# Optimization experiments

Hardware: AMD Instinct MI355X
Metric: run time of the kernel (lower is better)

The kernel has to match this reference:

```python
import jax, jax.numpy as jnp
import numpy as np

B, N, D, E = 64, 512, 256, 128   # batch, n_nodes, node_model_dim, edge_model_dim
N_ITERS = 20                      # max_iter_sinkhorn with fixed_n_iters=True


def setup_inputs() -> dict:
    key = jax.random.key(0)
    ks = jax.random.split(key, 9)
    return {
        "node_embeddings_inputs": jax.random.normal(ks[0], (B, N, D), jnp.float32),
        "node_masks_inputs": jax.random.randint(ks[1], (B, N), 0, 2).astype(bool),
        "node_embeddings_outputs": jax.random.normal(ks[2], (B, N, D), jnp.float32),
        # learned parameters
        "node_padding_features": jax.random.normal(ks[3], (1, 1, D), jnp.float32),
        "positional_encoding_outputs": jax.random.normal(ks[4], (1, N, D), jnp.float32),
        # stand-in for the (externally defined) EvoformerSetMatching pair stack:
        # a bilinear pair-affinity head, followed by the module's own linear_aff
        "W_a": jax.random.normal(ks[5], (D, E), jnp.float32) / np.sqrt(D),
        "W_b": jax.random.normal(ks[6], (D, E), jnp.float32) / np.sqrt(D),
        "w_aff": jax.random.normal(ks[7], (E,), jnp.float32) / np.sqrt(E),  # linear_aff weight
        "b_aff": jnp.zeros((), jnp.float32),                                # linear_aff bias
    }


def _sinkhorn(K, n_iters):
    # Fixed-iteration Sinkhorn projection toward a doubly-stochastic matrix:
    # alternately normalize columns (dim=2 sums) and rows (dim=1 sums).
    def step(P, _):
        P = P / jnp.sum(P, axis=2, keepdims=True)  # row-normalize over inputs axis
        P = P / jnp.sum(P, axis=1, keepdims=True)  # col-normalize over outputs axis
        return P, None
    P, _ = jax.lax.scan(step, K, None, length=n_iters)
    return P


def reference(node_embeddings_inputs, node_masks_inputs, node_embeddings_outputs,
              node_padding_features, positional_encoding_outputs,
              W_a, W_b, w_aff, b_aff):
    # replace padded input nodes with the learned padding feature
    mask = node_masks_inputs[..., None]                              # [B, N, 1]
    x_in = jnp.where(mask, node_padding_features, node_embeddings_inputs)
    # add positional encoding to output nodes (add_positionnal_outputs=True)
    x_out = node_embeddings_outputs + positional_encoding_outputs

    # pairwise affinity: aff[b, i(out), j(in)]  (linear_aff fused into the contraction
    # so the [B,N,N,E] pair tensor is never materialized)
    a = (x_out @ W_a) * w_aff                                        # [B, N, E]
    b = x_in @ W_b                                                   # [B, N, E]
    aff = jnp.einsum('bie,bje->bij', a, b) + b_aff                   # [B, N, N]

    # approximate doubly-stochastic init: average of the two marginal softmaxes
    K = 0.5 * jax.nn.softmax(aff, axis=1) + 0.5 * jax.nn.softmax(aff, axis=2)
    return _sinkhorn(K, N_ITERS)
```

## Files before the change

### kernel.cpp

```cpp
#include <hip/hip_runtime.h>
#include <cstddef>

static constexpr int CB = 64;
static constexpr int CN = 512;
static constexpr int CD = 256;
static constexpr int CE = 128;
static constexpr int CIT = 20;

typedef _Float16 half_t;
typedef __attribute__((ext_vector_type(8))) _Float16 v8h;
typedef __attribute__((ext_vector_type(4))) _Float16 v4h;
typedef __attribute__((ext_vector_type(4))) float v4f;

__device__ __forceinline__ void store_dual(v4f* l2p, v4f* llcp, v4f v) {
  asm volatile("global_store_dwordx4 %0, %2, off sc0\n\t"
               "global_store_dwordx4 %1, %2, off sc0 sc1"
               :: "v"(l2p), "v"(llcp), "v"(v) : "memory");
}
__device__ __forceinline__ void poll6(const v4f* a0, const v4f* a1,
                                      const v4f* a2, const v4f* c0,
                                      const v4f* c1, const v4f* c2,
                                      v4f& x0, v4f& x1, v4f& x2,
                                      v4f& y0, v4f& y1, v4f& y2) {
  asm volatile("global_load_dwordx4 %0, %6, off sc0\n\t"
               "global_load_dwordx4 %1, %7, off sc0\n\t"
               "global_load_dwordx4 %2, %8, off sc0\n\t"
               "global_load_dwordx4 %3, %9, off sc0 sc1\n\t"
               "global_load_dwordx4 %4, %10, off sc0 sc1\n\t"
               "global_load_dwordx4 %5, %11, off sc0 sc1\n\t"
               "s_waitcnt vmcnt(0)"
               : "=&v"(x0), "=&v"(x1), "=&v"(x2),
                 "=&v"(y0), "=&v"(y1), "=&v"(y2)
               : "v"(a0), "v"(a1), "v"(a2), "v"(c0), "v"(c1), "v"(c2)
               : "memory");
}
__device__ __forceinline__ bool allpos(v4f v) {
  return v[0] > 0.0f && v[1] > 0.0f && v[2] > 0.0f && v[3] > 0.0f;
}

__global__ __launch_bounds__(512) void k0_init(
    const void* __restrict__ mask, int* __restrict__ flag,
    const float* __restrict__ W_a, const float* __restrict__ W_b,
    const float* __restrict__ w_aff,
    half_t* __restrict__ WaF, half_t* __restrict__ WbF,
    float4* __restrict__ clearp, int nclear4) {
  const int tid = threadIdx.x;
  const int blk = blockIdx.x;
  if (blk == 1) return;
  if (blk >= 18) {
    const int idx = (blk - 18) * 512 + tid;
    if (idx < nclear4)
      clearp[idx] = make_float4(-1.0f, -1.0f, -1.0f, -1.0f);
    return;
  }
  if (blk >= 2) {
    const bool is_a = (blk < 10);
    const float* W = is_a ? W_a : W_b;
    half_t* WF = is_a ? WaF : WbF;
    const int e = (blk - (is_a ? 2 : 10)) * 512 + tid;
    const int fB = e >> 6, lane = e & 63;
    const int nn = fB >> 3, kf = fB & 7;
    const int col = nn * 16 + (lane & 15);
    const int q = lane >> 4;
    const float scale = is_a ? w_aff[col] : 1.0f;
    v8h hv;
#pragma unroll
    for (int j = 0; j < 8; ++j) {
      const int k = kf * 32 + q * 8 + j;
      hv[j] = (half_t)(W[(size_t)k * CE + col] * scale);
    }
    *(v8h*)&WF[(size_t)e * 8] = hv;
    return;
  }
  __shared__ int cnt[5];
  if (tid < 5) cnt[tid] = 0;
  __syncthreads();
  const unsigned char* p = (const unsigned char*)mask;
  int l0 = 0, l1 = 0, l2 = 0, l3 = 0, l4 = 0;
  const int base = tid * 64;
  for (int k = 0; k < 64; ++k) {
    const int off = base + k;
    if (p[off]) {
      const int m4 = off & 3;
      if (m4 == 1) l1++;
      else if (m4 == 2) l2++;
      else if (m4 == 3) l3++;
      else if ((off & 7) == 4) l4++;
      else l0++;
    }
  }
  if (l0) atomicAdd(&cnt[0], 1);
  if (l1) atomicAdd(&cnt[1], 1);
  if (l2) atomicAdd(&cnt[2], 1);
  if (l3) atomicAdd(&cnt[3], 1);
  if (l4) atomicAdd(&cnt[4], 1);
  __syncthreads();
  if (tid == 0) {
    int f;
    if (cnt[1]) f = 1;
    else if (cnt[2] || cnt[3]) f = 2;
    else if (cnt[4]) f = 0;
    else if (cnt[0]) f = 3;
    else f = 1;
    *flag = f;
  }
}

__global__ __launch_bounds__(256) void prep_both(
    const float* __restrict__ out_emb, const float* __restrict__ pos,
    const float* __restrict__ in_emb, const float* __restrict__ pad,
    const void* __restrict__ maskp, const int* __restrict__ flagp,
    const half_t* __restrict__ WaF, const half_t* __restrict__ WbF,
    half_t* __restrict__ A_h, half_t* __restrict__ Bm_h) {
  __shared__ half_t Xs[64][264];
  const int tid = threadIdx.x;
  const int wv = tid >> 6, ln = tid & 63;
  const bool isA = blockIdx.x < 512;
  const int row0 = (isA ? blockIdx.x : blockIdx.x - 512) * 64;
  const float* X = isA ? out_emb : in_emb;
  const float* extra = isA ? pos : pad;
  const half_t* Wfrag = isA ? WaF : WbF;
  half_t* out = isA ? A_h : Bm_h;
  const int flag = isA ? 0 : *flagp;

#pragma unroll 4
  for (int it = 0; it < 16; ++it) {
    const int r = it * 4 + wv;
    const int row = row0 + r;
    const int c = ln * 4;
    float4 x4;
    if (isA) {
      x4 = *(const float4*)&X[(size_t)row * CD + c];
      const int i = row & (CN - 1);
      const float4 p4 = *(const float4*)&extra[(size_t)i * CD + c];
      x4.x += p4.x; x4.y += p4.y; x4.z += p4.z; x4.w += p4.w;
    } else {
      bool m;
      if (flag == 1)      m = ((const unsigned char*)maskp)[row] != 0;
      else if (flag == 2) m = ((const float*)maskp)[row] != 0.0f;
      else if (flag == 3) m = ((const long long*)maskp)[row] != 0;
      else                m = ((const int*)maskp)[row] != 0;
      if (m) x4 = *(const float4*)&extra[c];
      else   x4 = *(const float4*)&X[(size_t)row * CD + c];
    }
    v4h hv;
    hv[0] = (half_t)x4.x; hv[1] = (half_t)x4.y;
    hv[2] = (half_t)x4.z; hv[3] = (half_t)x4.w;
    *(v4h*)&Xs[r][c] = hv;
  }
  __syncthreads();

  const int q = ln >> 4, l = ln & 15;
  v8h af[8];
#pragma unroll
  for (int kf = 0; kf < 8; ++kf)
    af[kf] = *(v8h*)&Xs[wv * 16 + l][kf * 32 + q * 8];
  v4f acc[8] = {};
#pragma unroll
  for (int nn = 0; nn < 8; ++nn) {
    v8h bf[8];
#pragma unroll
    for (int kf = 0; kf < 8; ++kf)
      bf[kf] = *(const v8h*)&Wfrag[(size_t)((nn * 8 + kf) * 64 + ln) * 8];
#pragma unroll
    for (int kf = 0; kf < 8; ++kf)
      acc[nn] = __builtin_amdgcn_mfma_f32_16x16x32_f16(af[kf], bf[kf], acc[nn], 0, 0, 0);
  }
#pragma unroll
  for (int nn = 0; nn < 8; ++nn)
#pragma unroll
    for (int g = 0; g < 4; ++g) {
      const int row = row0 + wv * 16 + q * 4 + g;
      out[(size_t)row * CE + nn * 16 + l] = (half_t)acc[nn][g];
    }
}

__global__ __launch_bounds__(512, 2) void fused_reg(
    const half_t* __restrict__ A_h, const half_t* __restrict__ B_h,
    const float* __restrict__ baff, float* __restrict__ P,
    float* __restrict__ partInit, float* __restrict__ partIter,
    float* __restrict__ partInitL2, float* __restrict__ partIterL2) {
  __shared__ float comb2[8][512][2];
  __shared__ __align__(16) float2 w12[512];
  __shared__ __align__(16) float QsL[512];
  __shared__ __align__(16) v4f csinv4[128];
  __shared__ __align__(16) half_t wAll[1056];

  const int tid = threadIdx.x;
  const int wv = tid >> 6, ln = tid & 63;
  const int q = ln >> 4, l = ln & 15;
  const int b = blockIdx.x & 63;
  const int slab = blockIdx.x >> 6;
  const int i0 = slab * 128;
  const float bbs = *baff - 2.7725887f;

  int rs3[3];
  {
    int k = 0;
#pragma unroll
    for (int sl = 0; sl < 4; ++sl)
      if (sl != slab) rs3[k++] = sl;
  }

  v8h af[4];
  {
    const half_t* Arow = &A_h[((size_t)b * CN + i0 + wv * 16 + l) * CE];
#pragma unroll
    for (int ki = 0; ki < 4; ++ki)
      af[ki] = *(const v8h*)&Arow[ki * 32 + q * 8];
  }
  v4h eh[32];
  v4h ehT[32];
  const half_t* Bbase = &B_h[(size_t)b * CN * CE];
#pragma unroll
  for (int ct = 0; ct < 32; ++ct) {
    v8h bf[4];
    const half_t* Brow = &Bbase[(size_t)(ct * 16 + l) * CE];
#pragma unroll
    for (int ki = 0; ki < 4; ++ki)
      bf[ki] = *(const v8h*)&Brow[ki * 32 + q * 8];
    v4f acc = {}, accT = {};
#pragma unroll
    for (int ki = 0; ki < 4; ++ki) {
      acc  = __builtin_amdgcn_mfma_f32_16x16x32_f16(af[ki], bf[ki], acc,  0, 0, 0);
      accT = __builtin_amdgcn_mfma_f32_16x16x32_f16(bf[ki], af[ki], accT, 0, 0, 0);
    }
#pragma unroll
    for (int g = 0; g < 4; ++g) {
      eh[ct][g]  = (half_t)__expf(acc[g]  + bbs);
      ehT[ct][g] = (half_t)__expf(accT[g] + bbs);
    }
  }

  v4h ones;
  ones[0] = (half_t)1.0f; ones[1] = (half_t)1.0f;
  ones[2] = (half_t)1.0f; ones[3] = (half_t)1.0f;
  v4f rowacc0 = {}, rowacc1 = {};
#pragma unroll
  for (int ct = 0; ct < 32; ct += 2) {
    const v4f c0 = __builtin_amdgcn_mfma_f32_16x16x16f16(ones, eh[ct], (v4f){}, 0, 0, 0);
    const v4f c1 = __builtin_amdgcn_mfma_f32_16x16x16f16(ones, eh[ct + 1], (v4f){}, 0, 0, 0);
    if (ln < 16) {
      comb2[wv][ct * 16 + ln][0] = c0[0];
      comb2[wv][(ct + 1) * 16 + ln][0] = c1[0];
    }
    rowacc0 = __builtin_amdgcn_mfma_f32_16x16x16f16(ones, ehT[ct],     rowacc0, 0, 0, 0);
    rowacc1 = __builtin_amdgcn_mfma_f32_16x16x16f16(ones, ehT[ct + 1], rowacc1, 0, 0, 0);
  }
  const float rowtot = rowacc0[0] + rowacc1[0];
  float rv[4];
#pragma unroll
  for (int g = 0; g < 4; ++g)
    rv[g] = 1.0f / __shfl(rowtot, q * 4 + g);
  __syncthreads();

  {
    float S = 0.0f;
#pragma unroll
    for (int w = 0; w < 8; ++w) S += comb2[w][tid][0];
    QsL[tid] = S;
  }
  __syncthreads();
  if (tid < 128) {
    const v4f s4 = *(const v4f*)&QsL[tid * 4];
    v4f* piL = (v4f*)partInitL2 + (size_t)b * 4 * 128;
    v4f* piC = (v4f*)partInit   + (size_t)b * 4 * 128;
    store_dual(&piL[slab * 128 + tid], &piC[slab * 128 + tid], s4);
    const v4f* a0 = &piL[rs3[0] * 128 + tid];
    const v4f* a1 = &piL[rs3[1] * 128 + tid];
    const v4f* a2 = &piL[rs3[2] * 128 + tid];
    const v4f* c0 = &piC[rs3[0] * 128 + tid];
    const v4f* c1 = &piC[rs3[1] * 128 + tid];
    const v4f* c2 = &piC[rs3[2] * 128 + tid];
    v4f s0, s1, s2;
    bool g0 = false, g1 = false, g2 = false;
    while (true) {
      v4f x0, x1, x2, y0, y1, y2;
      poll6(a0, a1, a2, c0, c1, c2, x0, x1, x2, y0, y1, y2);
      if (!g0) { if (allpos(x0)) { s0 = x0; g0 = true; } else if (allpos(y0)) { s0 = y0; g0 = true; } }
      if (!g1) { if (allpos(x1)) { s1 = x1; g1 = true; } else if (allpos(y1)) { s1 = y1; g1 = true; } }
      if (!g2) { if (allpos(x2)) { s2 = x2; g2 = true; } else if (allpos(y2)) { s2 = y2; g2 = true; } }
      if (g0 && g1 && g2) break;
      __builtin_amdgcn_s_sleep(1);
    }
    const v4f T = s4 + s0 + s1 + s2;
    v4f ci;
    v4h w1v, w2v;
#pragma unroll
    for (int j = 0; j < 4; ++j) {
      ci[j] = 1.0f / T[j];
      w1v[j] = (half_t)(0.5f * ci[j]);
      w2v[j] = (half_t)1.0f;
    }
    csinv4[tid] = ci;
    *(v4h*)&wAll[tid * 4] = w1v;
    *(v4h*)&wAll[544 + tid * 4] = w2v;
  }
  __syncthreads();
  const float ci0 = ((const float*)csinv4)[tid];

  const half_t* wbase = (l == 1) ? (wAll + 544) : wAll;
  float u_[4], uri[4];
  for (int t = 0; t < CIT; ++t) {
    __syncthreads();
    v4f Pe = {}, Po = {};
#pragma unroll
    for (int ct = 0; ct < 32; ct += 2) {
      const v4h wf0 = *(const v4h*)&wbase[ct * 16 + q * 4];
      const v4h wf1 = *(const v4h*)&wbase[(ct + 1) * 16 + q * 4];
      Pe = __builtin_amdgcn_mfma_f32_16x16x16f16(wf0, ehT[ct],     Pe, 0, 0, 0);
      Po = __builtin_amdgcn_mfma_f32_16x16x16f16(wf1, ehT[ct + 1], Po, 0, 0, 0);
    }
    const float Prow1 = Pe[0] + Po[0];
    const float Prow2 = Pe[1] + Po[1];
    v4h u_h, uri_h;
#pragma unroll
    for (int g = 0; g < 4; ++g) {
      const float p1 = __shfl(Prow1, q * 4 + g);
      const float p2 = __shfl(Prow2, q * 4 + g);
      u_[g] = 1.0f / (p1 + 0.5f * rv[g] * p2);
      uri[g] = u_[g] * rv[g];
      u_h[g] = (half_t)u_[g];
      uri_h[g] = (half_t)uri[g];
    }
    const v4h a2 = (l == 1) ? uri_h : u_h;
#pragma unroll
    for (int ct = 0; ct < 32; ++ct) {
      const v4f s = __builtin_amdgcn_mfma_f32_16x16x16f16(a2, eh[ct], (v4f){}, 0, 0, 0);
      if (ln < 16)
        *(float2*)&comb2[wv][ct * 16 + ln][0] = make_float2(s[0], s[1]);
    }
    __syncthreads();
    {
      float S1 = 0.0f, S2 = 0.0f;
#pragma unroll
      for (int w = 0; w < 8; ++w) {
        const float2 c2v = *(const float2*)&comb2[w][tid][0];
        S1 += c2v.x;
        S2 += c2v.y;
      }
      QsL[tid] = 0.5f * fmaf(ci0, S1, S2);
    }
    __syncthreads();
    if (tid < 128) {
      const v4f Q4 = *(const v4f*)&QsL[tid * 4];
      v4f* prL = (v4f*)partIterL2 + (((size_t)t * 64 + b) * 4) * 128;
      v4f* prC = (v4f*)partIter   + (((size_t)t * 64 + b) * 4) * 128;
      store_dual(&prL[slab * 128 + tid], &prC[slab * 128 + tid], Q4);
      const v4f* a0 = &prL[rs3[0] * 128 + tid];
      const v4f* a1 = &prL[rs3[1] * 128 + tid];
      const v4f* a2p = &prL[rs3[2] * 128 + tid];
      const v4f* c0 = &prC[rs3[0] * 128 + tid];
      const v4f* c1 = &prC[rs3[1] * 128 + tid];
      const v4f* c2 = &prC[rs3[2] * 128 + tid];
      v4f s0, s1, s2;
      bool g0 = false, g1 = false, g2 = false;
      while (true) {
        v4f x0, x1, x2, y0, y1, y2;
        poll6(a0, a1, a2p, c0, c1, c2, x0, x1, x2, y0, y1, y2);
        if (!g0) { if (allpos(x0)) { s0 = x0; g0 = true; } else if (allpos(y0)) { s0 = y0; g0 = true; } }
        if (!g1) { if (allpos(x1)) { s1 = x1; g1 = true; } else if (allpos(y1)) { s1 = y1; g1 = true; } }
        if (!g2) { if (allpos(x2)) { s2 = x2; g2 = true; } else if (allpos(y2)) { s2 = y2; g2 = true; } }
        if (g0 && g1 && g2) break;
        __builtin_amdgcn_s_sleep(1);
      }
      const v4f tot = Q4 + s0 + s1 + s2;
      const v4f ci = csinv4[tid];
      v4h w1v, w2v;
#pragma unroll
      for (int j = 0; j < 4; ++j) {
        const float vv = 1.0f / tot[j];
        w1v[j] = (half_t)(0.5f * vv * ci[j]);
        w2v[j] = (half_t)vv;
        if (t == CIT - 1)
          w12[tid * 4 + j] = make_float2(0.5f * vv * ci[j], vv);
      }
      *(v4h*)&wAll[tid * 4] = w1v;
      *(v4h*)&wAll[544 + tid * 4] = w2v;
    }
  }

  __syncthreads();
  float* Pb = &P[((size_t)b * CN + i0 + wv * 16 + q * 4) * CN];
#pragma unroll
  for (int ct = 0; ct < 32; ++ct) {
    const float2 w = w12[ct * 16 + l];
    const float c1 = w.x;
    const float c2 = 0.5f * w.y;
#pragma unroll
    for (int g = 0; g < 4; ++g) {
      const float e = (float)eh[ct][g];
      Pb[(size_t)g * CN + ct * 16 + l] = e * fmaf(u_[g], c1, uri[g] * c2);
    }
  }
}

extern "C" void kernel_launch(void* const* d_in, const int* in_sizes, int n_in,
                              void* d_out, int out_size, void* d_ws, size_t ws_size,
                              hipStream_t stream) {
  const float* in_emb  = (const float*)d_in[0];
  const void*  mask    = d_in[1];
  const float* out_emb = (const float*)d_in[2];
  const float* pad     = (const float*)d_in[3];
  const float* pos     = (const float*)d_in[4];
  const float* W_a     = (const float*)d_in[5];
  const float* W_b     = (const float*)d_in[6];
  const float* w_aff   = (const float*)d_in[7];
  const float* b_aff   = (const float*)d_in[8];
  float* P = (float*)d_out;

  char* ws = (char*)d_ws;
  const size_t MB = 1024 * 1024;
  const size_t KB = 1024;
  half_t* A_h  = (half_t*)ws;
  half_t* Bm_h = (half_t*)(ws + 8 * MB);
  int*    flag = (int*)(ws + 16 * MB);
  half_t* WaF  = (half_t*)(ws + 16 * MB + 16 * KB);
  half_t* WbF  = (half_t*)(ws + 16 * MB + 80 * KB);
  float* partInit   = (float*)(ws + 16 * MB + 256 * KB);
  float* partInitL2 = (float*)(ws + 16 * MB + 768 * KB);
  float* partIter   = (float*)(ws + 16 * MB + 1280 * KB);
  float* partIterL2 = (float*)(ws + 16 * MB + 1280 * KB + 10 * MB);

  const int nclear4 = (21 * 1024 * 1024) / 16;
  const int nclrblk = (nclear4 + 511) / 512;

  k0_init<<<dim3(18 + nclrblk), dim3(512), 0, stream>>>(
      mask, flag, W_a, W_b, w_aff, WaF, WbF, (float4*)partInit, nclear4);
  prep_both<<<dim3(1024), dim3(256), 0, stream>>>(
      out_emb, pos, in_emb, pad, mask, flag, WaF, WbF, A_h, Bm_h);
  fused_reg<<<dim3(256), dim3(512), 0, stream>>>(
      A_h, Bm_h, b_aff, P, partInit, partIter, partInitL2, partIterL2);
}
```

Baseline: 323.9 us.

## Co-locate batch slabs on one XCD and ring-buffer LLC partials with sign parity

Block indices are remapped so the four slab blocks of each batch share blockIdx mod 8. That likely places them on the same XCD, so the L2-coherent path of the cross-block partial-sum exchange can succeed instead of falling back to the slower LLC path. The LLC copy of the per-iteration partials becomes a two-slot ring. The sign alternates every two iterations, so stale data from two steps earlier can be told apart from fresh data. This shrinks the workspace region that k0_init must clear from 21 MB to 12 MB. The cost is a sign multiply and a parity-dependent check in the polling loop, and the scheme relies on partial sums being strictly positive.

```diff
diff --git a/kernel.cpp b/kernel.cpp
--- a/kernel.cpp
+++ b/kernel.cpp
@@ -12,10 +12,11 @@
 typedef __attribute__((ext_vector_type(4))) _Float16 v4h;
 typedef __attribute__((ext_vector_type(4))) float v4f;
 
-__device__ __forceinline__ void store_dual(v4f* l2p, v4f* llcp, v4f v) {
+__device__ __forceinline__ void store_dual2(v4f* l2p, v4f* llcp, v4f vpos,
+                                            v4f vsgn) {
   asm volatile("global_store_dwordx4 %0, %2, off sc0\n\t"
-               "global_store_dwordx4 %1, %2, off sc0 sc1"
-               :: "v"(l2p), "v"(llcp), "v"(v) : "memory");
+               "global_store_dwordx4 %1, %3, off sc0 sc1"
+               :: "v"(l2p), "v"(llcp), "v"(vpos), "v"(vsgn) : "memory");
 }
 __device__ __forceinline__ void poll6(const v4f* a0, const v4f* a1,
                                       const v4f* a2, const v4f* c0,
@@ -36,6 +37,9 @@
 }
 __device__ __forceinline__ bool allpos(v4f v) {
   return v[0] > 0.0f && v[1] > 0.0f && v[2] > 0.0f && v[3] > 0.0f;
+}
+__device__ __forceinline__ bool allneg(v4f v) {
+  return v[0] < 0.0f && v[1] < 0.0f && v[2] < 0.0f && v[3] < 0.0f;
 }
 
 __global__ __launch_bounds__(512) void k0_init(
@@ -178,8 +182,8 @@
 __global__ __launch_bounds__(512, 2) void fused_reg(
     const half_t* __restrict__ A_h, const half_t* __restrict__ B_h,
     const float* __restrict__ baff, float* __restrict__ P,
-    float* __restrict__ partInit, float* __restrict__ partIter,
-    float* __restrict__ partInitL2, float* __restrict__ partIterL2) {
+    float* __restrict__ partInit, float* __restrict__ partInitL2,
+    float* __restrict__ partIter, float* __restrict__ partIterL2) {
   __shared__ float comb2[8][512][2];
   __shared__ __align__(16) float2 w12[512];
   __shared__ __align__(16) float QsL[512];
@@ -189,8 +193,10 @@
   const int tid = threadIdx.x;
   const int wv = tid >> 6, ln = tid & 63;
   const int q = ln >> 4, l = ln & 15;
-  const int b = blockIdx.x & 63;
-  const int slab = blockIdx.x >> 6;
+  const int xcd = blockIdx.x & 7;
+  const int j_ = blockIdx.x >> 3;
+  const int b = ((j_ >> 2) << 3) | xcd;
+  const int slab = j_ & 3;
   const int i0 = slab * 128;
   const float bbs = *baff - 2.7725887f;
 
@@ -265,7 +271,7 @@
     const v4f s4 = *(const v4f*)&QsL[tid * 4];
     v4f* piL = (v4f*)partInitL2 + (size_t)b * 4 * 128;
     v4f* piC = (v4f*)partInit   + (size_t)b * 4 * 128;
-    store_dual(&piL[slab * 128 + tid], &piC[slab * 128 + tid], s4);
+    store_dual2(&piL[slab * 128 + tid], &piC[slab * 128 + tid], s4, s4);
     const v4f* a0 = &piL[rs3[0] * 128 + tid];
     const v4f* a1 = &piL[rs3[1] * 128 + tid];
     const v4f* a2 = &piL[rs3[2] * 128 + tid];
@@ -344,9 +350,13 @@
     __syncthreads();
     if (tid < 128) {
       const v4f Q4 = *(const v4f*)&QsL[tid * 4];
+      const int buf = t & 1;
+      const bool neg = ((t >> 1) & 1) != 0;
+      const float sgn = neg ? -1.0f : 1.0f;
+      const v4f Qs = Q4 * sgn;
       v4f* prL = (v4f*)partIterL2 + (((size_t)t * 64 + b) * 4) * 128;
-      v4f* prC = (v4f*)partIter   + (((size_t)t * 64 + b) * 4) * 128;
-      store_dual(&prL[slab * 128 + tid], &prC[slab * 128 + tid], Q4);
+      v4f* prC = (v4f*)partIter   + (((size_t)buf * 64 + b) * 4) * 128;
+      store_dual2(&prL[slab * 128 + tid], &prC[slab * 128 + tid], Q4, Qs);
       const v4f* a0 = &prL[rs3[0] * 128 + tid];
       const v4f* a1 = &prL[rs3[1] * 128 + tid];
       const v4f* a2p = &prL[rs3[2] * 128 + tid];
@@ -358,9 +368,12 @@
       while (true) {
         v4f x0, x1, x2, y0, y1, y2;
         poll6(a0, a1, a2p, c0, c1, c2, x0, x1, x2, y0, y1, y2);
-        if (!g0) { if (allpos(x0)) { s0 = x0; g0 = true; } else if (allpos(y0)) { s0 = y0; g0 = true; } }
-        if (!g1) { if (allpos(x1)) { s1 = x1; g1 = true; } else if (allpos(y1)) { s1 = y1; g1 = true; } }
-        if (!g2) { if (allpos(x2)) { s2 = x2; g2 = true; } else if (allpos(y2)) { s2 = y2; g2 = true; } }
+        if (!g0) { if (allpos(x0)) { s0 = x0; g0 = true; }
+                   else if (neg ? allneg(y0) : allpos(y0)) { s0 = y0 * sgn; g0 = true; } }
+        if (!g1) { if (allpos(x1)) { s1 = x1; g1 = true; }
+                   else if (neg ? allneg(y1) : allpos(y1)) { s1 = y1 * sgn; g1 = true; } }
+        if (!g2) { if (allpos(x2)) { s2 = x2; g2 = true; }
+                   else if (neg ? allneg(y2) : allpos(y2)) { s2 = y2 * sgn; g2 = true; } }
         if (g0 && g1 && g2) break;
         __builtin_amdgcn_s_sleep(1);
       }
@@ -417,12 +430,13 @@
   int*    flag = (int*)(ws + 16 * MB);
   half_t* WaF  = (half_t*)(ws + 16 * MB + 16 * KB);
   half_t* WbF  = (half_t*)(ws + 16 * MB + 80 * KB);
-  float* partInit   = (float*)(ws + 16 * MB + 256 * KB);
-  float* partInitL2 = (float*)(ws + 16 * MB + 768 * KB);
-  float* partIter   = (float*)(ws + 16 * MB + 1280 * KB);
-  float* partIterL2 = (float*)(ws + 16 * MB + 1280 * KB + 10 * MB);
-
-  const int nclear4 = (21 * 1024 * 1024) / 16;
+  char* slots = ws + 16 * MB + 256 * KB;
+  float* partInit   = (float*)(slots);
+  float* partInitL2 = (float*)(slots + 512 * KB);
+  float* partIter   = (float*)(slots + 1 * MB);
+  float* partIterL2 = (float*)(slots + 2 * MB);
+
+  const int nclear4 = (12 * 1024 * 1024) / 16;
   const int nclrblk = (nclear4 + 511) / 512;
 
   k0_init<<<dim3(18 + nclrblk), dim3(512), 0, stream>>>(
@@ -430,5 +444,5 @@
   prep_both<<<dim3(1024), dim3(256), 0, stream>>>(
       out_emb, pos, in_emb, pad, mask, flag, WaF, WbF, A_h, Bm_h);
   fused_reg<<<dim3(256), dim3(512), 0, stream>>>(
-      A_h, Bm_h, b_aff, P, partInit, partIter, partInitL2, partIterL2);
-}
+      A_h, Bm_h, b_aff, P, partInit, partInitL2, partIter, partIterL2);
+}
```

Measured after the change: 339.8 us. 1.05x slower.
